# Optimization experiments

Hardware: AMD Instinct MI355X
Metric: run time of the kernel (lower is better)

## Reference

```python
import jax, jax.numpy as jnp
import numpy as np
from jax.ops import segment_sum

N_NODES = 100000
N_EDGES = 1600000
IN_DIM, HID_DIM, OUT_DIM = 64, 48, 32


def setup_inputs() -> dict:
    key = jax.random.key(0)
    ks = jax.random.split(key, 4)
    x = jax.random.normal(ks[0], (N_NODES, IN_DIM), dtype=jnp.float32)
    edge_index = jax.random.randint(ks[1], (2, N_EDGES), 0, N_NODES, dtype=jnp.int64)
    W1 = jax.random.normal(ks[2], (IN_DIM, HID_DIM), dtype=jnp.float32) / np.sqrt(IN_DIM)
    b1 = jnp.zeros((HID_DIM,), dtype=jnp.float32)
    W2 = jax.random.normal(ks[3], (HID_DIM, OUT_DIM), dtype=jnp.float32) / np.sqrt(HID_DIM)
    b2 = jnp.zeros((OUT_DIM,), dtype=jnp.float32)
    return {"x": x, "edge_index": edge_index, "W1": W1, "b1": b1, "W2": W2, "b2": b2}


def _gcn_conv(x, W, b, src, dst, deg_inv_sqrt, n_nodes):
    # GCNConv: out = D^{-1/2} (A + I) D^{-1/2} (x W) + b
    h = x @ W                                   # [N, F_out]
    norm = deg_inv_sqrt[src] * deg_inv_sqrt[dst]  # [E+N]
    msg = h[src] * norm[:, None]                # gather + scale
    out = segment_sum(msg, dst, num_segments=n_nodes)  # scatter-add over dst
    return out + b


def reference(x, edge_index, W1, b1, W2, b2):
    n = x.shape[0]
    loop = jnp.arange(n, dtype=edge_index.dtype)
    src = jnp.concatenate([edge_index[0], loop])  # add self-loops (PyG default)
    dst = jnp.concatenate([edge_index[1], loop])
    deg = segment_sum(jnp.ones_like(dst, dtype=x.dtype), dst, num_segments=n)
    deg_inv_sqrt = jnp.where(deg > 0, jax.lax.rsqrt(jnp.maximum(deg, 1.0)), 0.0)
    h = _gcn_conv(x, W1, b1, src, dst, deg_inv_sqrt, n)
    h = jax.nn.relu(h)
    embeddings = _gcn_conv(h, W2, b2, src, dst, deg_inv_sqrt, n)
    return embeddings
```

## Files before the change

kernel.cpp:

```cpp
#include <hip/hip_runtime.h>
#include <hip/hip_fp16.h>


#define NN 100000
#define NE 1600000
#define NPB 128
#define NBUCK ((NN + NPB - 1) / NPB)
#define PBITS 17
#define PMASK ((1 << PBITS) - 1)
#define CHB 3
#define CHS 14
#define NKEY (NPB << CHB)
#define PART_B 512
#define EPT 8
#define PART_G ((NE + PART_B * EPT - 1) / (PART_B * EPT))
#define CAP 4096
#define UN 8

struct alignas(8)  half4 { __half2 lo, hi; };
struct alignas(16) half8 { __half2 a, b, c, d; };

__global__ void k_zero_b(int* __restrict__ bcnt) {
    int i = threadIdx.x;
    if (i < NBUCK) bcnt[i] = 0;
}

__global__ void k_hist(const int* __restrict__ dst, int* __restrict__ bcnt) {
    __shared__ int h[NBUCK];
    for (int i = threadIdx.x; i < NBUCK; i += blockDim.x) h[i] = 0;
    __syncthreads();
    int base = blockIdx.x * (PART_B * EPT);
    for (int k = 0; k < EPT; ++k) {
        int e = base + k * PART_B + threadIdx.x;
        if (e < NE) atomicAdd(&h[dst[e] >> 7], 1);
    }
    __syncthreads();
    for (int i = threadIdx.x; i < NBUCK; i += blockDim.x)
        if (h[i]) atomicAdd(&bcnt[i], h[i]);
}

__global__ void k_scan(const int* __restrict__ bcnt, int* __restrict__ bbase,
                       int* __restrict__ gcursor, int* __restrict__ row_ptr) {
    __shared__ int sm[1024];
    int t = threadIdx.x;
    int v = (t < NBUCK) ? bcnt[t] : 0;
    sm[t] = v; __syncthreads();
    for (int off = 1; off < 1024; off <<= 1) {
        int xv = (t >= off) ? sm[t - off] : 0;
        __syncthreads();
        sm[t] += xv;
        __syncthreads();
    }
    if (t < NBUCK) { int ex = sm[t] - v; bbase[t] = ex; gcursor[t] = ex; }
    if (t == 0) { bbase[NBUCK] = NE; row_ptr[NN] = NE; }
}

__global__ void k_part(const int* __restrict__ src, const int* __restrict__ dst,
                       int* __restrict__ gcursor, int* __restrict__ packed) {
    __shared__ int h[NBUCK];
    __shared__ int base[NBUCK];
    for (int i = threadIdx.x; i < NBUCK; i += blockDim.x) h[i] = 0;
    __syncthreads();
    int ebase = blockIdx.x * (PART_B * EPT);
    for (int k = 0; k < EPT; ++k) {
        int e = ebase + k * PART_B + threadIdx.x;
        if (e < NE) atomicAdd(&h[dst[e] >> 7], 1);
    }
    __syncthreads();
    for (int i = threadIdx.x; i < NBUCK; i += blockDim.x) {
        int c = h[i];
        if (c) base[i] = atomicAdd(&gcursor[i], c);
        h[i] = 0;
    }
    __syncthreads();
    for (int k = 0; k < EPT; ++k) {
        int e = ebase + k * PART_B + threadIdx.x;
        if (e < NE) {
            int d = dst[e];
            int b = d >> 7;
            int r = atomicAdd(&h[b], 1);
            packed[base[b] + r] = src[e] | ((d & (NPB - 1)) << PBITS);
        }
    }
}

__global__ void k_bsort(const int* __restrict__ packed, const int* __restrict__ bbase,
                        int* __restrict__ srcsort, int* __restrict__ row_ptr,
                        float* __restrict__ dinv) {
    __shared__ int stage[CAP];
    __shared__ int cnt[NKEY];
    __shared__ int tsum[256];
    int tid = threadIdx.x, b = blockIdx.x;
    int e0 = bbase[b], e1 = bbase[b + 1], sz = e1 - e0;
    for (int i = tid; i < NKEY; i += 256) cnt[i] = 0;
    __syncthreads();
    for (int i = tid; i < sz; i += 256) {
        int w = packed[e0 + i];
        if (i < CAP) stage[i] = w;
        int key = ((w >> PBITS) << CHB) | ((w & PMASK) >> CHS);
        atomicAdd(&cnt[key], 1);
    }
    __syncthreads();
    int k0 = tid * 4;
    int c0 = cnt[k0], c1 = cnt[k0 + 1], c2 = cnt[k0 + 2], c3 = cnt[k0 + 3];
    int loc = c0 + c1 + c2 + c3;
    tsum[tid] = loc;
    __syncthreads();
    for (int off = 1; off < 256; off <<= 1) {
        int v = (tid >= off) ? tsum[tid - off] : 0;
        __syncthreads();
        tsum[tid] += v;
        __syncthreads();
    }
    int base = tsum[tid] - loc;
    cnt[k0]     = base;
    cnt[k0 + 1] = base + c0;
    cnt[k0 + 2] = base + c0 + c1;
    cnt[k0 + 3] = base + c0 + c1 + c2;
    __syncthreads();
    if (tid < NPB) {
        int node = b * NPB + tid;
        int rs = cnt[tid << CHB];
        int re = (tid == NPB - 1) ? sz : cnt[(tid + 1) << CHB];
        if (node < NN) {
            row_ptr[node] = e0 + rs;
            dinv[node] = rsqrtf((float)(re - rs + 1));
        }
    }
    __syncthreads();
    for (int i = tid; i < sz; i += 256) {
        int w = (i < CAP) ? stage[i] : packed[e0 + i];
        int key = ((w >> PBITS) << CHB) | ((w & PMASK) >> CHS);
        int p = atomicAdd(&cnt[key], 1);
        srcsort[e0 + p] = w & PMASK;
    }
}

template <int K, int NC, int CPT, bool RELU_IN>
__global__ __launch_bounds__(256) void
k_gemm(const float* __restrict__ X, const float* __restrict__ W,
       const float* __restrict__ bin, const float* __restrict__ dinv,
       __half* __restrict__ Hh, int M) {
    constexpr int CG = NC / CPT;
    constexpr int MT = (256 / CG) * 2;
    constexpr int KF4 = K / 4;
    __shared__ float w[K * NC];
    __shared__ float bb[K];
    int tid = threadIdx.x;
    int R0 = blockIdx.x * MT;
    for (int i = tid; i < K * NC; i += 256) w[i] = W[i];
    if (RELU_IN)
        for (int i = tid; i < K; i += 256) bb[i] = bin[i];
    __syncthreads();

    int tc = tid % CG, tr = tid / CG;
    int r0 = R0 + 2 * tr, r1 = r0 + 1;
    int c0 = tc * CPT;
    bool ok0 = r0 < M, ok1 = r1 < M;
    const float4* X4 = (const float4*)X;
    const float4 z4 = make_float4(0.f, 0.f, 0.f, 0.f);

    float acc[2][CPT];
#pragma unroll
    for (int rr = 0; rr < 2; ++rr)
#pragma unroll
        for (int j = 0; j < CPT; ++j) acc[rr][j] = 0.f;

#pragma unroll 2
    for (int k4 = 0; k4 < KF4; ++k4) {
        float4 xa = ok0 ? X4[(size_t)r0 * KF4 + k4] : z4;
        float4 xb = ok1 ? X4[(size_t)r1 * KF4 + k4] : z4;
        float ar[4] = {xa.x, xa.y, xa.z, xa.w};
        float br[4] = {xb.x, xb.y, xb.z, xb.w};
#pragma unroll
        for (int j = 0; j < 4; ++j) {
            float va = ar[j], vb = br[j];
            if (RELU_IN) {
                float bv = bb[4 * k4 + j];
                va = fmaxf(va + bv, 0.f);
                vb = fmaxf(vb + bv, 0.f);
            }
#pragma unroll
            for (int q = 0; q < CPT / 4; ++q) {
                float4 wv = *(const float4*)&w[(4 * k4 + j) * NC + c0 + 4 * q];
                acc[0][q*4+0] = fmaf(va, wv.x, acc[0][q*4+0]);
                acc[0][q*4+1] = fmaf(va, wv.y, acc[0][q*4+1]);
                acc[0][q*4+2] = fmaf(va, wv.z, acc[0][q*4+2]);
                acc[0][q*4+3] = fmaf(va, wv.w, acc[0][q*4+3]);
                acc[1][q*4+0] = fmaf(vb, wv.x, acc[1][q*4+0]);
                acc[1][q*4+1] = fmaf(vb, wv.y, acc[1][q*4+1]);
                acc[1][q*4+2] = fmaf(vb, wv.z, acc[1][q*4+2]);
                acc[1][q*4+3] = fmaf(vb, wv.w, acc[1][q*4+3]);
            }
        }
    }
#pragma unroll
    for (int rr = 0; rr < 2; ++rr) {
        int gr = r0 + rr;
        if (gr >= M) continue;
        float d = dinv[gr];
#pragma unroll
        for (int q = 0; q < CPT / 4; ++q) {
            __half2 p0 = __floats2half2_rn(acc[rr][q*4+0] * d, acc[rr][q*4+1] * d);
            __half2 p1 = __floats2half2_rn(acc[rr][q*4+2] * d, acc[rr][q*4+3] * d);
            half4 hv; hv.lo = p0; hv.hi = p1;
            *(half4*)(Hh + (size_t)gr * NC + c0 + 4 * q) = hv;
        }
    }
}

template <int NC, bool BIAS>
__global__ void k_agg(const __half* __restrict__ Hh, const int* __restrict__ row_ptr,
                      const int* __restrict__ srcsort, const float* __restrict__ dinv,
                      const float* __restrict__ bias, float* __restrict__ out) {
    constexpr int Q = NC / 8;
    int idx = blockIdx.x * blockDim.x + threadIdx.x;
    if (idx >= NN * Q) return;
    int r = idx / Q, q = idx - r * Q;
    half8 sv = *(const half8*)(Hh + (size_t)r * NC + 8 * q);
    float2 f0 = __half22float2(sv.a), f1 = __half22float2(sv.b);
    float2 f2 = __half22float2(sv.c), f3 = __half22float2(sv.d);
    float a0 = f0.x, a1 = f0.y, a2 = f1.x, a3 = f1.y;
    float a4 = f2.x, a5 = f2.y, a6 = f3.x, a7 = f3.y;
    int e0 = row_ptr[r], e1 = row_ptr[r + 1];
    int e = e0;
    for (; e + UN <= e1; e += UN) {
        int ss[UN];
#pragma unroll
        for (int u = 0; u < UN; ++u) ss[u] = srcsort[e + u];
        half8 vv[UN];
#pragma unroll
        for (int u = 0; u < UN; ++u)
            vv[u] = *(const half8*)(Hh + (size_t)ss[u] * NC + 8 * q);
#pragma unroll
        for (int u = 0; u < UN; ++u) {
            float2 g0 = __half22float2(vv[u].a), g1 = __half22float2(vv[u].b);
            float2 g2 = __half22float2(vv[u].c), g3 = __half22float2(vv[u].d);
            a0 += g0.x; a1 += g0.y; a2 += g1.x; a3 += g1.y;
            a4 += g2.x; a5 += g2.y; a6 += g3.x; a7 += g3.y;
        }
    }
    for (; e < e1; ++e) {
        int s = srcsort[e];
        half8 v = *(const half8*)(Hh + (size_t)s * NC + 8 * q);
        float2 g0 = __half22float2(v.a), g1 = __half22float2(v.b);
        float2 g2 = __half22float2(v.c), g3 = __half22float2(v.d);
        a0 += g0.x; a1 += g0.y; a2 += g1.x; a3 += g1.y;
        a4 += g2.x; a5 += g2.y; a6 += g3.x; a7 += g3.y;
    }
    float d = dinv[r];
    a0 *= d; a1 *= d; a2 *= d; a3 *= d; a4 *= d; a5 *= d; a6 *= d; a7 *= d;
    if (BIAS) {
        const float4* b4 = (const float4*)bias;
        float4 bv0 = b4[2 * q], bv1 = b4[2 * q + 1];
        a0 += bv0.x; a1 += bv0.y; a2 += bv0.z; a3 += bv0.w;
        a4 += bv1.x; a5 += bv1.y; a6 += bv1.z; a7 += bv1.w;
    }
    float4* o4 = (float4*)(out + (size_t)r * NC + 8 * q);
    o4[0] = make_float4(a0, a1, a2, a3);
    o4[1] = make_float4(a4, a5, a6, a7);
}

extern "C" void kernel_launch(void* const* d_in, const int* in_sizes, int n_in,
                              void* d_out, int out_size, void* d_ws, size_t ws_size,
                              hipStream_t stream) {
    const float* x  = (const float*)d_in[0];
    const int*   ei = (const int*)d_in[1];
    const float* W1 = (const float*)d_in[2];
    const float* b1 = (const float*)d_in[3];
    const float* W2 = (const float*)d_in[4];
    const float* b2 = (const float*)d_in[5];
    float* out = (float*)d_out;

    const int* src = ei;
    const int* dst = ei + NE;

    char* p = (char*)d_ws;
    auto take = [&](size_t elems) { void* q = p; p += ((elems * 4 + 255) & ~255ull); return q; };
    int*    bcnt    = (int*)take(NBUCK);
    int*    bbase   = (int*)take(NBUCK + 1);
    int*    gcursor = (int*)take(NBUCK);
    int*    row_ptr = (int*)take(NN + 1);
    float*  dinv    = (float*)take(NN);
    int*    srcsort = (int*)take(NE);
    __half* Hh      = (__half*)take((size_t)NN * 24);
    float*  agg1    = (float*)take((size_t)NN * 48);
    int*    packed  = (int*)agg1;
    __half* Hh2     = Hh;

    const int B = 256;
    const int GB = (NN + 127) / 128;
    k_zero_b<<<1, 1024, 0, stream>>>(bcnt);
    k_hist<<<PART_G, PART_B, 0, stream>>>(dst, bcnt);
    k_scan<<<1, 1024, 0, stream>>>(bcnt, bbase, gcursor, row_ptr);
    k_part<<<PART_G, PART_B, 0, stream>>>(src, dst, gcursor, packed);
    k_bsort<<<NBUCK, 256, 0, stream>>>(packed, bbase, srcsort, row_ptr, dinv);

    k_gemm<64, 48, 12, false><<<GB, 256, 0, stream>>>(x, W1, nullptr, dinv, Hh, NN);
    k_agg<48, false><<<(NN * 6 + B - 1) / B, B, 0, stream>>>(Hh, row_ptr, srcsort, dinv, nullptr, agg1);

    k_gemm<48, 32, 8, true><<<GB, 256, 0, stream>>>(agg1, W2, b1, dinv, Hh2, NN);
    k_agg<32, true><<<(NN * 4 + B - 1) / B, B, 0, stream>>>(Hh2, row_ptr, srcsort, dinv, b2, out);
}
```

Measured before the change: 235.7 us.

## Fuse layer-1 aggregation with bias, ReLU and layer-2 GEMM in shared memory

Replaces the separate layer-1 aggregation and layer-2 GEMM kernels with one kernel. It aggregates 128 rows into shared memory, applies bias and ReLU, then multiplies by W2 and writes the fp16 features for layer 2. This removes the round trip of the 48-wide fp32 intermediate through global memory and one kernel launch. The cost is that each block's gather work is spread over fewer threads per row tile, which may reduce latency hiding. The packed buffer is now allocated separately and reused for Hh2.

```diff
diff --git a/kernel.cpp b/kernel.cpp
--- a/kernel.cpp
+++ b/kernel.cpp
@@ -136,21 +136,17 @@
     }
 }
 
-template <int K, int NC, int CPT, bool RELU_IN>
+template <int K, int NC, int CPT>
 __global__ __launch_bounds__(256) void
 k_gemm(const float* __restrict__ X, const float* __restrict__ W,
-       const float* __restrict__ bin, const float* __restrict__ dinv,
-       __half* __restrict__ Hh, int M) {
+       const float* __restrict__ dinv, __half* __restrict__ Hh, int M) {
     constexpr int CG = NC / CPT;
     constexpr int MT = (256 / CG) * 2;
     constexpr int KF4 = K / 4;
     __shared__ float w[K * NC];
-    __shared__ float bb[K];
     int tid = threadIdx.x;
     int R0 = blockIdx.x * MT;
     for (int i = tid; i < K * NC; i += 256) w[i] = W[i];
-    if (RELU_IN)
-        for (int i = tid; i < K; i += 256) bb[i] = bin[i];
     __syncthreads();
 
     int tc = tid % CG, tr = tid / CG;
@@ -175,11 +171,6 @@
 #pragma unroll
         for (int j = 0; j < 4; ++j) {
             float va = ar[j], vb = br[j];
-            if (RELU_IN) {
-                float bv = bb[4 * k4 + j];
-                va = fmaxf(va + bv, 0.f);
-                vb = fmaxf(vb + bv, 0.f);
-            }
 #pragma unroll
             for (int q = 0; q < CPT / 4; ++q) {
                 float4 wv = *(const float4*)&w[(4 * k4 + j) * NC + c0 + 4 * q];
@@ -209,7 +200,107 @@
     }
 }
 
-template <int NC, bool BIAS>
+__global__ __launch_bounds__(256) void
+k_fused48(const __half* __restrict__ Hh, const int* __restrict__ row_ptr,
+          const int* __restrict__ srcsort, const float* __restrict__ dinv,
+          const float* __restrict__ b1, const float* __restrict__ W2,
+          __half* __restrict__ Hh2) {
+    constexpr int ROWS = 128, XS = 49;
+    __shared__ float Xs[ROWS * XS];
+    __shared__ float w2[48 * 32];
+    __shared__ float bb[48];
+    int tid = threadIdx.x;
+    int R0 = blockIdx.x * ROWS;
+    for (int i = tid; i < 48 * 32; i += 256) w2[i] = W2[i];
+    if (tid < 48) bb[tid] = b1[tid];
+    __syncthreads();
+
+    for (int t = tid; t < ROWS * 6; t += 256) {
+        int lr = t / 6, q = t - lr * 6;
+        int r = R0 + lr;
+        if (r >= NN) continue;
+        half8 sv = *(const half8*)(Hh + (size_t)r * 48 + 8 * q);
+        float2 f0 = __half22float2(sv.a), f1 = __half22float2(sv.b);
+        float2 f2 = __half22float2(sv.c), f3 = __half22float2(sv.d);
+        float a0 = f0.x, a1 = f0.y, a2 = f1.x, a3 = f1.y;
+        float a4 = f2.x, a5 = f2.y, a6 = f3.x, a7 = f3.y;
+        int e0 = row_ptr[r], e1 = row_ptr[r + 1];
+        int e = e0;
+        for (; e + UN <= e1; e += UN) {
+            int ss[UN];
+#pragma unroll
+            for (int u = 0; u < UN; ++u) ss[u] = srcsort[e + u];
+            half8 vv[UN];
+#pragma unroll
+            for (int u = 0; u < UN; ++u)
+                vv[u] = *(const half8*)(Hh + (size_t)ss[u] * 48 + 8 * q);
+#pragma unroll
+            for (int u = 0; u < UN; ++u) {
+                float2 g0 = __half22float2(vv[u].a), g1 = __half22float2(vv[u].b);
+                float2 g2 = __half22float2(vv[u].c), g3 = __half22float2(vv[u].d);
+                a0 += g0.x; a1 += g0.y; a2 += g1.x; a3 += g1.y;
+                a4 += g2.x; a5 += g2.y; a6 += g3.x; a7 += g3.y;
+            }
+        }
+        for (; e < e1; ++e) {
+            int s = srcsort[e];
+            half8 v = *(const half8*)(Hh + (size_t)s * 48 + 8 * q);
+            float2 g0 = __half22float2(v.a), g1 = __half22float2(v.b);
+            float2 g2 = __half22float2(v.c), g3 = __half22float2(v.d);
+            a0 += g0.x; a1 += g0.y; a2 += g1.x; a3 += g1.y;
+            a4 += g2.x; a5 += g2.y; a6 += g3.x; a7 += g3.y;
+        }
+        float d = dinv[r];
+        float* xr = &Xs[lr * XS + 8 * q];
+        const float* bf = &bb[8 * q];
+        xr[0] = fmaxf(fmaf(a0, d, bf[0]), 0.f);
+        xr[1] = fmaxf(fmaf(a1, d, bf[1]), 0.f);
+        xr[2] = fmaxf(fmaf(a2, d, bf[2]), 0.f);
+        xr[3] = fmaxf(fmaf(a3, d, bf[3]), 0.f);
+        xr[4] = fmaxf(fmaf(a4, d, bf[4]), 0.f);
+        xr[5] = fmaxf(fmaf(a5, d, bf[5]), 0.f);
+        xr[6] = fmaxf(fmaf(a6, d, bf[6]), 0.f);
+        xr[7] = fmaxf(fmaf(a7, d, bf[7]), 0.f);
+    }
+    __syncthreads();
+
+    int tc = tid & 3, tr = tid >> 2;
+    int r0l = 2 * tr, c0 = tc * 8;
+    float acc[2][8];
+#pragma unroll
+    for (int rr = 0; rr < 2; ++rr)
+#pragma unroll
+        for (int j = 0; j < 8; ++j) acc[rr][j] = 0.f;
+#pragma unroll 4
+    for (int k = 0; k < 48; ++k) {
+        float x0 = Xs[r0l * XS + k];
+        float x1 = Xs[(r0l + 1) * XS + k];
+        float4 wv0 = *(const float4*)&w2[k * 32 + c0];
+        float4 wv1 = *(const float4*)&w2[k * 32 + c0 + 4];
+        acc[0][0] = fmaf(x0, wv0.x, acc[0][0]); acc[0][1] = fmaf(x0, wv0.y, acc[0][1]);
+        acc[0][2] = fmaf(x0, wv0.z, acc[0][2]); acc[0][3] = fmaf(x0, wv0.w, acc[0][3]);
+        acc[0][4] = fmaf(x0, wv1.x, acc[0][4]); acc[0][5] = fmaf(x0, wv1.y, acc[0][5]);
+        acc[0][6] = fmaf(x0, wv1.z, acc[0][6]); acc[0][7] = fmaf(x0, wv1.w, acc[0][7]);
+        acc[1][0] = fmaf(x1, wv0.x, acc[1][0]); acc[1][1] = fmaf(x1, wv0.y, acc[1][1]);
+        acc[1][2] = fmaf(x1, wv0.z, acc[1][2]); acc[1][3] = fmaf(x1, wv0.w, acc[1][3]);
+        acc[1][4] = fmaf(x1, wv1.x, acc[1][4]); acc[1][5] = fmaf(x1, wv1.y, acc[1][5]);
+        acc[1][6] = fmaf(x1, wv1.z, acc[1][6]); acc[1][7] = fmaf(x1, wv1.w, acc[1][7]);
+    }
+#pragma unroll
+    for (int rr = 0; rr < 2; ++rr) {
+        int gr = R0 + r0l + rr;
+        if (gr >= NN) continue;
+        float d = dinv[gr];
+        __half2 p0 = __floats2half2_rn(acc[rr][0] * d, acc[rr][1] * d);
+        __half2 p1 = __floats2half2_rn(acc[rr][2] * d, acc[rr][3] * d);
+        __half2 p2 = __floats2half2_rn(acc[rr][4] * d, acc[rr][5] * d);
+        __half2 p3 = __floats2half2_rn(acc[rr][6] * d, acc[rr][7] * d);
+        half8 hv; hv.a = p0; hv.b = p1; hv.c = p2; hv.d = p3;
+        *(half8*)(Hh2 + (size_t)gr * 32 + c0) = hv;
+    }
+}
+
+template <int NC>
 __global__ void k_agg(const __half* __restrict__ Hh, const int* __restrict__ row_ptr,
                       const int* __restrict__ srcsort, const float* __restrict__ dinv,
                       const float* __restrict__ bias, float* __restrict__ out) {
@@ -249,13 +340,12 @@
         a4 += g2.x; a5 += g2.y; a6 += g3.x; a7 += g3.y;
     }
     float d = dinv[r];
-    a0 *= d; a1 *= d; a2 *= d; a3 *= d; a4 *= d; a5 *= d; a6 *= d; a7 *= d;
-    if (BIAS) {
-        const float4* b4 = (const float4*)bias;
-        float4 bv0 = b4[2 * q], bv1 = b4[2 * q + 1];
-        a0 += bv0.x; a1 += bv0.y; a2 += bv0.z; a3 += bv0.w;
-        a4 += bv1.x; a5 += bv1.y; a6 += bv1.z; a7 += bv1.w;
-    }
+    const float4* b4 = (const float4*)bias;
+    float4 bv0 = b4[2 * q], bv1 = b4[2 * q + 1];
+    a0 = fmaf(a0, d, bv0.x); a1 = fmaf(a1, d, bv0.y);
+    a2 = fmaf(a2, d, bv0.z); a3 = fmaf(a3, d, bv0.w);
+    a4 = fmaf(a4, d, bv1.x); a5 = fmaf(a5, d, bv1.y);
+    a6 = fmaf(a6, d, bv1.z); a7 = fmaf(a7, d, bv1.w);
     float4* o4 = (float4*)(out + (size_t)r * NC + 8 * q);
     o4[0] = make_float4(a0, a1, a2, a3);
     o4[1] = make_float4(a4, a5, a6, a7);
@@ -284,9 +374,8 @@
     float*  dinv    = (float*)take(NN);
     int*    srcsort = (int*)take(NE);
     __half* Hh      = (__half*)take((size_t)NN * 24);
-    float*  agg1    = (float*)take((size_t)NN * 48);
-    int*    packed  = (int*)agg1;
-    __half* Hh2     = Hh;
+    int*    packed  = (int*)take(NE);
+    __half* Hh2     = (__half*)packed;
 
     const int B = 256;
     const int GB = (NN + 127) / 128;
@@ -296,9 +385,7 @@
     k_part<<<PART_G, PART_B, 0, stream>>>(src, dst, gcursor, packed);
     k_bsort<<<NBUCK, 256, 0, stream>>>(packed, bbase, srcsort, row_ptr, dinv);
 
-    k_gemm<64, 48, 12, false><<<GB, 256, 0, stream>>>(x, W1, nullptr, dinv, Hh, NN);
-    k_agg<48, false><<<(NN * 6 + B - 1) / B, B, 0, stream>>>(Hh, row_ptr, srcsort, dinv, nullptr, agg1);
-
-    k_gemm<48, 32, 8, true><<<GB, 256, 0, stream>>>(agg1, W2, b1, dinv, Hh2, NN);
-    k_agg<32, true><<<(NN * 4 + B - 1) / B, B, 0, stream>>>(Hh2, row_ptr, srcsort, dinv, b2, out);
-}
+    k_gemm<64, 48, 12><<<GB, 256, 0, stream>>>(x, W1, dinv, Hh, NN);
+    k_fused48<<<GB, 256, 0, stream>>>(Hh, row_ptr, srcsort, dinv, b1, W2, Hh2);
+    k_agg<32><<<(NN * 4 + B - 1) / B, B, 0, stream>>>(Hh2, row_ptr, srcsort, dinv, b2, out);
+}
```

Result: faster. 222.6 us (-5.5%).
